# Optimization experiments

Measured on AMD Instinct MI355X. Metric: run time of the kernel, lower is better.

Reference implementation:

```python
import jax, jax.numpy as jnp
import numpy as np

B, S, DIM = 2, 2048, 2048
H, KV = 16, 8
HD = DIM // H          # 128 head_dim
N_REP = H // KV        # 2


def _rope(x, cos, sin):
    # x: (B,S,h,HD) with interleaved (real, imag) pairs along last dim
    xr = x[..., 0::2]                      # (B,S,h,HD/2)
    xi = x[..., 1::2]
    cos = cos[None, :, None, :]            # (1,S,1,HD/2)
    sin = sin[None, :, None, :]
    or_ = xr * cos - xi * sin
    oi_ = xr * sin + xi * cos
    return jnp.stack([or_, oi_], axis=-1).reshape(x.shape)


def setup_inputs() -> dict:
    key = jax.random.key(0)
    ks = jax.random.split(key, 5)
    x = jax.random.normal(ks[0], (B, S, DIM), dtype=jnp.float32)
    # RoPE tables: theta = 10000, half = HD/2
    inv_freq = 1.0 / (10000.0 ** (np.arange(0, HD, 2, dtype=np.float32) / HD))
    t = np.arange(S, dtype=np.float32)
    ang = np.outer(t, inv_freq)                           # (S, HD/2)
    freqs_cos = jnp.asarray(np.cos(ang), dtype=jnp.float32)
    freqs_sin = jnp.asarray(np.sin(ang), dtype=jnp.float32)
    sc = 0.02
    wq = jax.random.normal(ks[1], (DIM, H * HD), dtype=jnp.float32) * sc
    wk = jax.random.normal(ks[2], (DIM, KV * HD), dtype=jnp.float32) * sc
    wv = jax.random.normal(ks[3], (DIM, KV * HD), dtype=jnp.float32) * sc
    wo = jax.random.normal(ks[4], (DIM, DIM), dtype=jnp.float32) * sc
    return {"x": x, "freqs_cos": freqs_cos, "freqs_sin": freqs_sin,
            "wq": wq, "wk": wk, "wv": wv, "wo": wo}


def reference(x, freqs_cos, freqs_sin, wq, wk, wv, wo):
    b, s, _ = x.shape
    xq = (x @ wq).reshape(b, s, H, HD)
    xk = (x @ wk).reshape(b, s, KV, HD)
    xv = (x @ wv).reshape(b, s, KV, HD)
    xq = _rope(xq, freqs_cos, freqs_sin)
    xk = _rope(xk, freqs_cos, freqs_sin)
    # GQA: repeat kv heads n_rep times along head axis
    xk = jnp.repeat(xk, N_REP, axis=2)     # (b,s,H,HD)
    xv = jnp.repeat(xv, N_REP, axis=2)
    scores = jnp.einsum('bqhd,bkhd->bhqk', xq, xk) / jnp.sqrt(
        jnp.asarray(HD, dtype=x.dtype))
    mask = jnp.triu(jnp.full((s, s), -jnp.inf, dtype=x.dtype), k=1)
    attn = jax.nn.softmax(scores + mask[None, None, :, :], axis=-1)
    out = jnp.einsum('bhqk,bkhd->bqhd', attn, xv).reshape(b, s, DIM)
    return out @ wo
```

## Files before the change

### kernel.cpp

```cpp
#include <hip/hip_runtime.h>

typedef unsigned short u16;
typedef short bf16x8 __attribute__((ext_vector_type(8)));
typedef float f32x4 __attribute__((ext_vector_type(4)));
typedef float f32x16 __attribute__((ext_vector_type(16)));
typedef int i32x2 __attribute__((ext_vector_type(2)));
typedef unsigned int u32x4 __attribute__((ext_vector_type(4)));
typedef unsigned short u16x4 __attribute__((ext_vector_type(4)));
typedef unsigned short u16x8 __attribute__((ext_vector_type(8)));

#define S_LEN 2048
#define NHEAD 16
#define NKV 8
#define HD 128

__device__ __forceinline__ u16 f2bf(float f) {
  unsigned u = __builtin_bit_cast(unsigned, f);
  u = (u + 0x7FFFu + ((u >> 16) & 1u)) >> 16;
  return (u16)u;
}
__device__ __forceinline__ float bf2f(u16 h) {
  unsigned u = ((unsigned)h) << 16;
  return __builtin_bit_cast(float, u);
}

__device__ __forceinline__ void gl_lds16(const void* g, void* l) {
  __builtin_amdgcn_global_load_lds(
      (const __attribute__((address_space(1))) unsigned int*)g,
      (__attribute__((address_space(3))) unsigned int*)l, 16, 0, 0);
}

__device__ __forceinline__ unsigned cvtpk_bf16(float a, float b) {
  unsigned r;
  asm("v_cvt_pk_bf16_f32 %0, %1, %2" : "=v"(r) : "v"(a), "v"(b));
  return r;
}

__global__ __launch_bounds__(256) void conv_bf16(const float* __restrict__ in,
                                                 u16* __restrict__ out, int n4) {
  int i = blockIdx.x * 256 + threadIdx.x;
  if (i >= n4) return;
  f32x4 v = *(const f32x4*)(in + (size_t)i * 4);
  u16x4 o;
#pragma unroll
  for (int j = 0; j < 4; ++j) o[j] = f2bf(v[j]);
  *(u16x4*)(out + (size_t)i * 4) = o;
}

__global__ __launch_bounds__(256) void transpose_w4(
    const float* __restrict__ wq, const float* __restrict__ wk,
    const float* __restrict__ wv, const float* __restrict__ wo,
    u16* __restrict__ wcatT, u16* __restrict__ woT) {
  __shared__ float tile[64][65];
  int id = blockIdx.x;
  const float* in;
  u16* out;
  int N, roff, nx;
  if (id < 1024) {
    in = wq; out = wcatT; N = 2048; roff = 0; nx = 32;
  } else if (id < 1536) {
    in = wk; out = wcatT; N = 1024; roff = 2048; nx = 16; id -= 1024;
  } else if (id < 2048) {
    in = wv; out = wcatT; N = 1024; roff = 3072; nx = 16; id -= 1536;
  } else {
    in = wo; out = woT; N = 2048; roff = 0; nx = 32; id -= 2048;
  }
  int bx = id % nx;
  int by = id / nx;
  int k0 = by * 64, n0 = bx * 64;
  int tx = threadIdx.x & 63, ty = threadIdx.x >> 6;
#pragma unroll
  for (int p = 0; p < 16; ++p) {
    int r = p * 4 + ty;
    tile[r][tx] = in[(size_t)(k0 + r) * N + n0 + tx];
  }
  __syncthreads();
#pragma unroll
  for (int p = 0; p < 16; ++p) {
    int r = p * 4 + ty;
    out[(size_t)(roff + n0 + r) * 2048 + k0 + tx] = f2bf(tile[tx][r]);
  }
}

__global__ __launch_bounds__(256) void rope_qk(u16* __restrict__ q, u16* __restrict__ k,
                                               const float* __restrict__ fc,
                                               const float* __restrict__ fs) {
  const int QC = 2 * NHEAD * S_LEN * HD / 8;
  const int KC = 2 * NKV * S_LEN * HD / 8;
  int i = blockIdx.x * 256 + threadIdx.x;
  if (i >= QC + KC) return;
  u16* base;
  float scale;
  size_t e;
  if (i < QC) {
    base = q;
    e = (size_t)i * 8;
    scale = 0.12751744540368598f;
  } else {
    base = k;
    e = (size_t)(i - QC) * 8;
    scale = 1.0f;
  }
  int d8 = (int)(e & 127);
  int s = (int)((e >> 7) & (S_LEN - 1));
  int dp0 = d8 >> 1;
  u16x8 v = *(const u16x8*)(base + e);
  u16x8 o;
#pragma unroll
  for (int p = 0; p < 4; ++p) {
    float xr = bf2f(v[2 * p]), xi = bf2f(v[2 * p + 1]);
    float c = fc[s * 64 + dp0 + p], sn = fs[s * 64 + dp0 + p];
    o[2 * p] = f2bf((xr * c - xi * sn) * scale);
    o[2 * p + 1] = f2bf((xr * sn + xi * c) * scale);
  }
  *(u16x8*)(base + e) = o;
}

template <int EPI>
__global__ __launch_bounds__(512, 2) void gemm8p(
    const u16* __restrict__ A, const u16* __restrict__ Bt, float* __restrict__ Cf,
    u16* __restrict__ Qo, u16* __restrict__ Ko, u16* __restrict__ Vo, int N, int ntn) {
  constexpr int K = 2048, NH = K / 32;
  __shared__ __align__(16) u16 lds[4][256 * 64];

  const int t = threadIdx.x;
  const int l = t & 63, lh = l >> 4, ll = l & 15;
  const int w = t >> 6, wm = w >> 2, wn = w & 3;

  const int bid = blockIdx.x;
  const int swz = (bid & 7) * (gridDim.x >> 3) + (bid >> 3);
  const int tm = swz / ntn, tn = swz % ntn;

  const u16* Ab = A + (size_t)tm * 256 * K;
  const u16* Bb = Bt + (size_t)tn * 256 * K;

  const int srow = t >> 3;
  const int sphys = t & 7;
  const int slog = sphys ^ (srow & 7);
  const u16* sbase = (slog < 4) ? Ab : Bb;
  const int scol = (slog & 3) * 8;

  f32x4 acc[8][4] = {};

  auto STAGE = [&](int H) {
    u16* buf = &lds[H & 3][0];
    const u16* sp = sbase + (size_t)srow * K + H * 32 + scol;
#pragma unroll
    for (int c = 0; c < 4; ++c)
      gl_lds16(sp + (size_t)c * 64 * K, buf + c * 4096 + t * 8);
  };

  auto BODY = [&](int H) {
    const u16* buf = &lds[H & 3][0];
    bf16x8 af[8], bv[4];
#pragma unroll
    for (int i = 0; i < 8; ++i) {
      int row = wm * 128 + i * 16 + ll;
      af[i] = *(const bf16x8*)(buf + row * 64 + (lh ^ (ll & 7)) * 8);
    }
#pragma unroll
    for (int n = 0; n < 4; ++n) {
      int row = wn * 64 + n * 16 + ll;
      bv[n] = *(const bf16x8*)(buf + row * 64 + ((4 + lh) ^ (ll & 7)) * 8);
    }
    __builtin_amdgcn_s_setprio(1);
#pragma unroll
    for (int i = 0; i < 8; ++i)
#pragma unroll
      for (int n = 0; n < 4; ++n)
        acc[i][n] =
            __builtin_amdgcn_mfma_f32_16x16x32_bf16(af[i], bv[n], acc[i][n], 0, 0, 0);
    __builtin_amdgcn_s_setprio(0);
  };

  STAGE(0);
  STAGE(1);
  STAGE(2);
  __builtin_amdgcn_s_waitcnt(0xF70 | 8);
  __builtin_amdgcn_s_barrier();
  asm volatile("" ::: "memory");

  for (int H = 0; H < NH - 3; ++H) {
    STAGE(H + 3);
    BODY(H);
    __builtin_amdgcn_s_waitcnt(0xF70 | 8);
    __builtin_amdgcn_s_barrier();
    asm volatile("" ::: "memory");
  }
  BODY(NH - 3);
  __builtin_amdgcn_s_waitcnt(0xF70 | 4);
  __builtin_amdgcn_s_barrier();
  asm volatile("" ::: "memory");
  BODY(NH - 2);
  __builtin_amdgcn_s_waitcnt(0xF70);
  __builtin_amdgcn_s_barrier();
  asm volatile("" ::: "memory");
  BODY(NH - 1);

#pragma unroll
  for (int i = 0; i < 8; ++i)
#pragma unroll
    for (int n = 0; n < 4; ++n)
#pragma unroll
      for (int j = 0; j < 4; ++j) {
        int row = tm * 256 + wm * 128 + i * 16 + lh * 4 + j;
        int col = tn * 256 + wn * 64 + n * 16 + ll;
        if constexpr (EPI == 0) {
          Cf[(size_t)row * N + col] = acc[i][n][j];
        } else {
          int b = row >> 11, s = row & (S_LEN - 1);
          u16 val = f2bf(acc[i][n][j]);
          int d = col & 127;
          if (col < 2048) {
            int hh = col >> 7;
            Qo[(((size_t)b * NHEAD + hh) * S_LEN + s) * HD + d] = val;
          } else if (col < 3072) {
            int kh = (col >> 7) & 7;
            Ko[(((size_t)b * NKV + kh) * S_LEN + s) * HD + d] = val;
          } else {
            int kh = (col >> 7) & 7;
            Vo[(((size_t)b * NKV + kh) * S_LEN + s) * HD + d] = val;
          }
        }
      }
}

__global__ __launch_bounds__(256) void transpose_v(const u16* __restrict__ V,
                                                   u16* __restrict__ Vt) {
  __shared__ u16 tile[64][72];
  int id = blockIdx.x;
  int bkv = id >> 6;
  int dt = (id >> 5) & 1;
  int st = id & 31;
  const u16* Vb = V + (size_t)bkv * S_LEN * HD;
  u16* Vo = Vt + (size_t)bkv * HD * S_LEN;
  int r = threadIdx.x >> 3, c8 = (threadIdx.x & 7) * 8;
#pragma unroll
  for (int it = 0; it < 2; ++it) {
    int rr = it * 32 + r;
    *(u16x8*)(&tile[rr][c8]) =
        *(const u16x8*)(Vb + (size_t)(st * 64 + rr) * HD + dt * 64 + c8);
  }
  __syncthreads();
#pragma unroll
  for (int it = 0; it < 2; ++it) {
    int rr = it * 32 + r;
    u16x8 o;
#pragma unroll
    for (int j = 0; j < 8; ++j) o[j] = tile[c8 + j][rr];
    *(u16x8*)(Vo + (size_t)(dt * 64 + rr) * S_LEN + st * 64 + c8) = o;
  }
}

__global__ __launch_bounds__(256, 2) void attn_fwd(const u16* __restrict__ Q,
                                                   const u16* __restrict__ Kh,
                                                   const u16* __restrict__ Vt,
                                                   u16* __restrict__ O) {
  __shared__ __align__(16) u16 KS[2][64 * 128];
  __shared__ __align__(16) u16 VS[2][128 * 64];

  const int t = threadIdx.x;
  const int l = t & 63, hi = l >> 5, ll = l & 31;
  const int wq = t >> 6;

  const int bid = blockIdx.x;
  const int qt = 15 - (bid >> 5);
  const int bh = bid & 31;
  const int b = bh >> 4, h = bh & 15;
  const int bkv = b * NKV + (h >> 1);

  const u16* Qb = Q + (size_t)bh * S_LEN * HD;
  const u16* Kb = Kh + (size_t)bkv * S_LEN * HD;
  const u16* Vb = Vt + (size_t)bkv * HD * S_LEN;

  const int q0w = qt * 128 + wq * 32;
  const int qg = q0w + ll;

  bf16x8 qf[8];
#pragma unroll
  for (int c = 0; c < 8; ++c)
    qf[c] = *(const bf16x8*)(Qb + (size_t)qg * HD + c * 16 + hi * 8);

  const int krow = t >> 4, kslot = t & 15;
  const int vrow = t >> 3, vslot = t & 7;
  u16x8 krg[4], vrg[4];

  auto loadKV = [&](int tile) {
    const int kv0 = tile * 64;
#pragma unroll
    for (int c = 0; c < 4; ++c) {
      int r = c * 16 + krow;
      int sg = (kslot & 8) | ((kslot & 7) ^ (r & 7));
      krg[c] = *(const u16x8*)(Kb + (size_t)(kv0 + r) * HD + sg * 8);
    }
#pragma unroll
    for (int c = 0; c < 4; ++c) {
      int d = c * 32 + vrow;
      int sg = vslot ^ (d & 7);
      vrg[c] = *(const u16x8*)(Vb + (size_t)d * S_LEN + kv0 + sg * 8);
    }
  };
  auto storeKV = [&](int bi) {
#pragma unroll
    for (int c = 0; c < 4; ++c)
      *(u16x8*)(&KS[bi][(c * 16 + krow) * 128 + kslot * 8]) = krg[c];
#pragma unroll
    for (int c = 0; c < 4; ++c)
      *(u16x8*)(&VS[bi][(c * 32 + vrow) * 64 + vslot * 8]) = vrg[c];
  };

  f32x16 accO[4] = {};
  float m = -1e30f, lsum = 0.f;

  const int nt = 2 * qt + 2;
  loadKV(0);
  storeKV(0);
  __syncthreads();

  for (int tt = 0; tt < nt; ++tt) {
    const int kv0 = tt * 64;
    const bool actn = (tt + 1 < nt);
    if (actn) loadKV(tt + 1);

    if (kv0 <= q0w + 31) {
      const u16* ks = &KS[tt & 1][0];
      const u16* vs = &VS[tt & 1][0];

      f32x16 st[2] = {};
      __builtin_amdgcn_s_setprio(1);
#pragma unroll
      for (int c = 0; c < 8; ++c) {
        int slot = 2 * c + hi;
        int eff = (slot & 8) | ((slot & 7) ^ (ll & 7));
        bf16x8 kf0 = *(const bf16x8*)(ks + (size_t)ll * 128 + eff * 8);
        st[0] = __builtin_amdgcn_mfma_f32_32x32x16_bf16(kf0, qf[c], st[0], 0, 0, 0);
        bf16x8 kf1 = *(const bf16x8*)(ks + (size_t)(32 + ll) * 128 + eff * 8);
        st[1] = __builtin_amdgcn_mfma_f32_32x32x16_bf16(kf1, qf[c], st[1], 0, 0, 0);
      }
      __builtin_amdgcn_s_setprio(0);

      if (kv0 + 63 > q0w) {
#pragma unroll
        for (int f = 0; f < 2; ++f)
#pragma unroll
          for (int r = 0; r < 16; ++r) {
            int kvg = kv0 + f * 32 + (r & 3) + 8 * (r >> 2) + 4 * hi;
            if (kvg > qg) st[f][r] = -1e30f;
          }
      }

      float a[16];
#pragma unroll
      for (int i = 0; i < 16; ++i) a[i] = fmaxf(st[0][i], st[1][i]);
#pragma unroll
      for (int s = 8; s >= 1; s >>= 1)
#pragma unroll
        for (int i = 0; i < 8; ++i)
          if (i < s) a[i] = fmaxf(a[i], a[i + s]);
      float pmax = fmaxf(a[0], __shfl_xor(a[0], 32));

      if (tt == 0) {
        m = pmax;
      } else if (!__all(pmax <= m + 8.0f)) {
        float mnew = fmaxf(m, pmax);
        float corr = __builtin_amdgcn_exp2f(m - mnew);
        m = mnew;
        lsum *= corr;
        int ci = __builtin_bit_cast(int, corr);
#pragma unroll
        for (int reg = 0; reg < 16; ++reg) {
          int row = (reg & 3) + 8 * (reg >> 2) + 4 * hi;
          float cq = __builtin_bit_cast(
              float, __builtin_amdgcn_ds_bpermute(row << 2, ci));
#pragma unroll
          for (int dblk = 0; dblk < 4; ++dblk) accO[dblk][reg] *= cq;
        }
      }

#pragma unroll
      for (int f = 0; f < 2; ++f)
#pragma unroll
        for (int r = 0; r < 16; ++r)
          st[f][r] = __builtin_amdgcn_exp2f(st[f][r] - m);
      float s1[16];
#pragma unroll
      for (int i = 0; i < 16; ++i) s1[i] = st[0][i] + st[1][i];
#pragma unroll
      for (int s = 8; s >= 1; s >>= 1)
#pragma unroll
        for (int i = 0; i < 8; ++i)
          if (i < s) s1[i] += s1[i + s];
      lsum += s1[0];

      unsigned pk[8][2];
#pragma unroll
      for (int bg = 0; bg < 8; ++bg)
#pragma unroll
        for (int ap = 0; ap < 2; ++ap)
          pk[bg][ap] = cvtpk_bf16(st[bg >> 2][(bg & 3) * 4 + 2 * ap],
                                  st[bg >> 2][(bg & 3) * 4 + 2 * ap + 1]);

      __builtin_amdgcn_s_setprio(1);
#pragma unroll
      for (int kc = 0; kc < 4; ++kc) {
        i32x2 sa = __builtin_amdgcn_permlane32_swap(
            (int)pk[2 * kc][0], (int)pk[2 * kc + 1][0], false, false);
        i32x2 sb = __builtin_amdgcn_permlane32_swap(
            (int)pk[2 * kc][1], (int)pk[2 * kc + 1][1], false, false);
        union {
          unsigned u[4];
          bf16x8 v;
        } pa;
        pa.u[0] = (unsigned)sa[0];
        pa.u[1] = (unsigned)sb[0];
        pa.u[2] = (unsigned)sa[1];
        pa.u[3] = (unsigned)sb[1];
        int eff = (2 * kc + hi) ^ (ll & 7);
#pragma unroll
        for (int dblk = 0; dblk < 4; ++dblk) {
          bf16x8 vf = *(const bf16x8*)(vs + (size_t)(dblk * 32 + ll) * 64 + eff * 8);
          accO[dblk] =
              __builtin_amdgcn_mfma_f32_32x32x16_bf16(pa.v, vf, accO[dblk], 0, 0, 0);
        }
      }
      __builtin_amdgcn_s_setprio(0);
    }

    __syncthreads();
    if (actn) storeKV((tt + 1) & 1);
    __syncthreads();
  }

  lsum += __shfl_xor(lsum, 32);
  float linv = 1.0f / lsum;
  int li = __builtin_bit_cast(int, linv);
  float inv[16];
#pragma unroll
  for (int reg = 0; reg < 16; ++reg) {
    int row = (reg & 3) + 8 * (reg >> 2) + 4 * hi;
    inv[reg] = __builtin_bit_cast(float, __builtin_amdgcn_ds_bpermute(row << 2, li));
  }
#pragma unroll
  for (int dblk = 0; dblk < 4; ++dblk)
#pragma unroll
    for (int reg = 0; reg < 16; ++reg) {
      int row = (reg & 3) + 8 * (reg >> 2) + 4 * hi;
      O[(size_t)(b * S_LEN + q0w + row) * 2048 + h * HD + dblk * 32 + ll] =
          f2bf(accO[dblk][reg] * inv[reg]);
    }
}

extern "C" void kernel_launch(void* const* d_in, const int* in_sizes, int n_in,
                              void* d_out, int out_size, void* d_ws, size_t ws_size,
                              hipStream_t stream) {
  (void)in_sizes;
  (void)n_in;
  (void)out_size;
  (void)ws_size;
  const float* x = (const float*)d_in[0];
  const float* fc = (const float*)d_in[1];
  const float* fs = (const float*)d_in[2];
  const float* wq = (const float*)d_in[3];
  const float* wk = (const float*)d_in[4];
  const float* wv = (const float*)d_in[5];
  const float* wo = (const float*)d_in[6];
  float* out = (float*)d_out;

  char* ws = (char*)d_ws;
  u16* wcatT = (u16*)ws;
  u16* vtb = (u16*)ws;
  u16* woT = (u16*)(ws + 16777216);
  u16* xo = (u16*)(ws + 25165824);
  u16* qb = (u16*)(ws + 41943040);
  u16* kb = (u16*)(ws + 58720256);
  u16* vb = (u16*)(ws + 67108864);

  conv_bf16<<<8192, 256, 0, stream>>>(x, xo, 2097152);
  transpose_w4<<<3072, 256, 0, stream>>>(wq, wk, wv, wo, wcatT, woT);

  gemm8p<1><<<256, 512, 0, stream>>>(xo, wcatT, nullptr, qb, kb, vb, 4096, 16);
  transpose_v<<<1024, 256, 0, stream>>>(vb, vtb);
  rope_qk<<<6144, 256, 0, stream>>>(qb, kb, fc, fs);
  attn_fwd<<<512, 256, 0, stream>>>(qb, kb, vtb, xo);
  gemm8p<0><<<128, 512, 0, stream>>>(xo, woT, out, nullptr, nullptr, nullptr, 2048, 8);
}
```

Baseline: 223.8 us.

## Split GEMM k-step into two barrier-separated phases interleaving loads and MFMA

Restructures the bf16 GEMM main loop so each k-step runs in two halves. Each half loads half of the A fragments and issues half of the next stage's global-to-LDS copies, then runs 16 MFMAs under raised priority, with block barriers between phases to keep waves in lockstep. Launch bounds drop from 2 to 1 blocks per SM, so the compiler has more registers but occupancy is lower. The finer interleave is meant to overlap memory traffic with matrix math better, at the cost of extra barriers per iteration.

```diff
diff --git a/kernel.cpp b/kernel.cpp
--- a/kernel.cpp
+++ b/kernel.cpp
@@ -34,6 +34,12 @@
   unsigned r;
   asm("v_cvt_pk_bf16_f32 %0, %1, %2" : "=v"(r) : "v"(a), "v"(b));
   return r;
+}
+
+__device__ __forceinline__ void BAR() {
+  asm volatile("" ::: "memory");
+  __builtin_amdgcn_s_barrier();
+  asm volatile("" ::: "memory");
 }
 
 __global__ __launch_bounds__(256) void conv_bf16(const float* __restrict__ in,
@@ -117,7 +123,7 @@
 }
 
 template <int EPI>
-__global__ __launch_bounds__(512, 2) void gemm8p(
+__global__ __launch_bounds__(512, 1) void gemm8f(
     const u16* __restrict__ A, const u16* __restrict__ Bt, float* __restrict__ Cf,
     u16* __restrict__ Qo, u16* __restrict__ Ko, u16* __restrict__ Vo, int N, int ntn) {
   constexpr int K = 2048, NH = K / 32;
@@ -142,60 +148,64 @@
 
   f32x4 acc[8][4] = {};
 
-  auto STAGE = [&](int H) {
-    u16* buf = &lds[H & 3][0];
-    const u16* sp = sbase + (size_t)srow * K + H * 32 + scol;
-#pragma unroll
-    for (int c = 0; c < 4; ++c)
+  auto STAGE2 = [&](int h, int p) {
+    u16* buf = &lds[h & 3][0];
+    const u16* sp = sbase + (size_t)srow * K + h * 32 + scol;
+#pragma unroll
+    for (int c = 2 * p; c < 2 * p + 2; ++c)
       gl_lds16(sp + (size_t)c * 64 * K, buf + c * 4096 + t * 8);
   };
 
-  auto BODY = [&](int H) {
-    const u16* buf = &lds[H & 3][0];
-    bf16x8 af[8], bv[4];
-#pragma unroll
-    for (int i = 0; i < 8; ++i) {
-      int row = wm * 128 + i * 16 + ll;
-      af[i] = *(const bf16x8*)(buf + row * 64 + (lh ^ (ll & 7)) * 8);
+  STAGE2(0, 0); STAGE2(0, 1);
+  STAGE2(1, 0); STAGE2(1, 1);
+  STAGE2(2, 0); STAGE2(2, 1);
+  __builtin_amdgcn_s_waitcnt(0xF70 | 8);
+  BAR();
+
+  const int sw = ll & 7;
+  for (int h = 0; h < NH; ++h) {
+    const u16* buf = &lds[h & 3][0];
+    bf16x8 bv[4], af[4];
+#pragma unroll
+    for (int n = 0; n < 4; ++n)
+      bv[n] = *(const bf16x8*)(buf + (wn * 64 + n * 16 + ll) * 64 + (((4 + lh) ^ sw)) * 8);
+#pragma unroll
+    for (int m = 0; m < 4; ++m)
+      af[m] = *(const bf16x8*)(buf + (wm * 128 + m * 16 + ll) * 64 + ((lh ^ sw)) * 8);
+    if (h + 3 < NH) STAGE2(h + 3, 0);
+    BAR();
+    __builtin_amdgcn_s_setprio(1);
+#pragma unroll
+    for (int m = 0; m < 4; ++m)
+#pragma unroll
+      for (int n = 0; n < 4; ++n)
+        acc[m][n] =
+            __builtin_amdgcn_mfma_f32_16x16x32_bf16(af[m], bv[n], acc[m][n], 0, 0, 0);
+    __builtin_amdgcn_s_setprio(0);
+    BAR();
+#pragma unroll
+    for (int m = 0; m < 4; ++m)
+      af[m] = *(const bf16x8*)(buf + (wm * 128 + (4 + m) * 16 + ll) * 64 + ((lh ^ sw)) * 8);
+    if (h + 3 < NH) STAGE2(h + 3, 1);
+    BAR();
+    __builtin_amdgcn_s_setprio(1);
+#pragma unroll
+    for (int m = 0; m < 4; ++m)
+#pragma unroll
+      for (int n = 0; n < 4; ++n)
+        acc[4 + m][n] =
+            __builtin_amdgcn_mfma_f32_16x16x32_bf16(af[m], bv[n], acc[4 + m][n], 0, 0, 0);
+    __builtin_amdgcn_s_setprio(0);
+    if (h + 1 < NH) {
+      if (h + 3 < NH)
+        __builtin_amdgcn_s_waitcnt(0xF70 | 8);
+      else if (h + 3 == NH)
+        __builtin_amdgcn_s_waitcnt(0xF70 | 4);
+      else
+        __builtin_amdgcn_s_waitcnt(0xF70);
+      BAR();
     }
-#pragma unroll
-    for (int n = 0; n < 4; ++n) {
-      int row = wn * 64 + n * 16 + ll;
-      bv[n] = *(const bf16x8*)(buf + row * 64 + ((4 + lh) ^ (ll & 7)) * 8);
-    }
-    __builtin_amdgcn_s_setprio(1);
-#pragma unroll
-    for (int i = 0; i < 8; ++i)
-#pragma unroll
-      for (int n = 0; n < 4; ++n)
-        acc[i][n] =
-            __builtin_amdgcn_mfma_f32_16x16x32_bf16(af[i], bv[n], acc[i][n], 0, 0, 0);
-    __builtin_amdgcn_s_setprio(0);
-  };
-
-  STAGE(0);
-  STAGE(1);
-  STAGE(2);
-  __builtin_amdgcn_s_waitcnt(0xF70 | 8);
-  __builtin_amdgcn_s_barrier();
-  asm volatile("" ::: "memory");
-
-  for (int H = 0; H < NH - 3; ++H) {
-    STAGE(H + 3);
-    BODY(H);
-    __builtin_amdgcn_s_waitcnt(0xF70 | 8);
-    __builtin_amdgcn_s_barrier();
-    asm volatile("" ::: "memory");
-  }
-  BODY(NH - 3);
-  __builtin_amdgcn_s_waitcnt(0xF70 | 4);
-  __builtin_amdgcn_s_barrier();
-  asm volatile("" ::: "memory");
-  BODY(NH - 2);
-  __builtin_amdgcn_s_waitcnt(0xF70);
-  __builtin_amdgcn_s_barrier();
-  asm volatile("" ::: "memory");
-  BODY(NH - 1);
+  }
 
 #pragma unroll
   for (int i = 0; i < 8; ++i)
@@ -478,9 +488,9 @@
   conv_bf16<<<8192, 256, 0, stream>>>(x, xo, 2097152);
   transpose_w4<<<3072, 256, 0, stream>>>(wq, wk, wv, wo, wcatT, woT);
 
-  gemm8p<1><<<256, 512, 0, stream>>>(xo, wcatT, nullptr, qb, kb, vb, 4096, 16);
+  gemm8f<1><<<256, 512, 0, stream>>>(xo, wcatT, nullptr, qb, kb, vb, 4096, 16);
   transpose_v<<<1024, 256, 0, stream>>>(vb, vtb);
   rope_qk<<<6144, 256, 0, stream>>>(qb, kb, fc, fs);
   attn_fwd<<<512, 256, 0, stream>>>(qb, kb, vtb, xo);
-  gemm8p<0><<<128, 512, 0, stream>>>(xo, woT, out, nullptr, nullptr, nullptr, 2048, 8);
-}
+  gemm8f<0><<<128, 512, 0, stream>>>(xo, woT, out, nullptr, nullptr, nullptr, 2048, 8);
+}
```

Result: no change. 228.2 us (+2.0%).
